# Kernel tuning notes

Measured on AMD Instinct MI355X. Metric: run time of the kernel, lower is better.

The kernel has to match this reference:

```python
import jax, jax.numpy as jnp
import numpy as np

M1, M2, M3 = 12, 12, 8
WIDTH = 32


def _spectral_conv(v, wr, wi):
    # v: [B, C, X, Y, T]; wr/wi: [4, Ci, Co, M1, M2, M3]
    B, C, X, Y, T = v.shape
    vft = jnp.fft.rfftn(v, axes=(-3, -2, -1))  # [B,C,X,Y,T//2+1] complex
    w = wr.astype(jnp.complex64) + 1j * wi.astype(jnp.complex64)
    mul = lambda blk, ww: jnp.einsum('bixyz,ioxyz->boxyz', blk, ww)
    out = jnp.zeros((B, wr.shape[2], X, Y, T // 2 + 1), dtype=vft.dtype)
    out = out.at[:, :, :M1, :M2, :M3].set(mul(vft[:, :, :M1, :M2, :M3], w[0]))
    out = out.at[:, :, -M1:, :M2, :M3].set(mul(vft[:, :, -M1:, :M2, :M3], w[1]))
    out = out.at[:, :, :M1, -M2:, :M3].set(mul(vft[:, :, :M1, -M2:, :M3], w[2]))
    out = out.at[:, :, -M1:, -M2:, :M3].set(mul(vft[:, :, -M1:, -M2:, :M3], w[3]))
    return jnp.fft.irfftn(out, s=(X, Y, T), axes=(-3, -2, -1))


def _conv1x1(v, w, b):
    # v: [B,C,X,Y,T]; w: [Co,Ci]; b: [Co]
    return jnp.einsum('bixyz,oi->boxyz', v, w) + b[None, :, None, None, None]


def setup_inputs() -> dict:
    key = jax.random.key(0)
    ks = jax.random.split(key, 24)
    B, X, Y, T = 8, 64, 64, 40
    W = WIDTH
    scale = 1.0 / (W * W)
    d = {}
    d['h'] = jax.random.normal(ks[0], (B, X, Y, T, 2), dtype=jnp.float32)
    d['x'] = jax.random.normal(ks[1], (B, X, Y, T, 3), dtype=jnp.float32)
    d['fc0_w'] = jax.random.normal(ks[2], (5, W), dtype=jnp.float32) * 0.3
    d['fc0_b'] = jnp.zeros((W,), dtype=jnp.float32)
    for i, name in enumerate(['sc0', 'sc1', 'sc3']):
        d[name + '_wr'] = scale * jax.random.uniform(ks[3 + 2 * i], (4, W, W, M1, M2, M3), dtype=jnp.float32)
        d[name + '_wi'] = scale * jax.random.uniform(ks[4 + 2 * i], (4, W, W, M1, M2, M3), dtype=jnp.float32)
    for i, name in enumerate(['w0', 'w1', 'w3']):
        d[name + '_w'] = jax.random.normal(ks[9 + 2 * i], (W, W), dtype=jnp.float32) * (1.0 / np.sqrt(W))
        d[name + '_b'] = jnp.zeros((W,), dtype=jnp.float32)
    d['fc1_w'] = jax.random.normal(ks[15], (W, 64), dtype=jnp.float32) * (1.0 / np.sqrt(W))
    d['fc1_b'] = jnp.zeros((64,), dtype=jnp.float32)
    d['fc2_w'] = jax.random.normal(ks[16], (64, 2), dtype=jnp.float32) * 0.125
    d['fc2_b'] = jnp.zeros((2,), dtype=jnp.float32)
    return d


def reference(h, x, fc0_w, fc0_b, sc0_wr, sc0_wi, sc1_wr, sc1_wi, sc3_wr, sc3_wi,
              w0_w, w0_b, w1_w, w1_b, w3_w, w3_b, fc1_w, fc1_b, fc2_w, fc2_b):
    v = jnp.concatenate((h, x), axis=-1)                 # [B,X,Y,T,5]
    v = v @ fc0_w + fc0_b                                # lift to width
    v = jnp.transpose(v, (0, 4, 1, 2, 3))                # [B,W,X,Y,T]
    v = jax.nn.gelu(_spectral_conv(v, sc0_wr, sc0_wi) + _conv1x1(v, w0_w, w0_b), approximate=False)
    v = jax.nn.gelu(_spectral_conv(v, sc1_wr, sc1_wi) + _conv1x1(v, w1_w, w1_b), approximate=False)
    v = _spectral_conv(v, sc3_wr, sc3_wi) + _conv1x1(v, w3_w, w3_b)
    v = jnp.transpose(v, (0, 2, 3, 4, 1))                # [B,X,Y,T,W]
    v = jax.nn.gelu(v @ fc1_w + fc1_b, approximate=False)
    return v @ fc2_w + fc2_b                             # [B,X,Y,T,2]
```

## Files before the change

kernel.cpp:

```cpp
#include <hip/hip_runtime.h>
#include <math.h>

#define BATCH 8
#define WID   32
#define NX    64
#define NY    64
#define NT    40
#define M1C   12
#define KT    8
#define KXC   24
#define KYC   24
#define NXY   (NX*NY)
#define NXYT  (NXY*NT)
#define NP    (BATCH*NXYT)

#define TWO_PI 6.283185307179586f

static __device__ __forceinline__ float gelu_f(float v){
  return 0.5f*v*(1.0f + erff(v*0.7071067811865476f));
}

static __device__ __forceinline__ void barrier_lds(){
  asm volatile("s_waitcnt lgkmcnt(0)\n\ts_barrier" ::: "memory");
}


__global__ __launch_bounds__(256) void k_fc0(const float* __restrict__ h, const float* __restrict__ x,
                                             const float* __restrict__ w, const float* __restrict__ b,
                                             float* __restrict__ V){
  __shared__ float sw[160], sb[32];
  int tid=threadIdx.x;
  if(tid<160) sw[tid]=w[tid];
  if(tid<32)  sb[tid]=b[tid];
  __syncthreads();
  int pl = tid>>3, q = tid&7;
  int p = blockIdx.x*32 + pl;
  float i0=h[(size_t)p*2], i1=h[(size_t)p*2+1];
  float i2=x[(size_t)p*3], i3=x[(size_t)p*3+1], i4=x[(size_t)p*3+2];
  int c0=q*4;
  float4 o;
  float* po=(float*)&o;
  #pragma unroll
  for(int u=0;u<4;u++){
    int c=c0+u;
    po[u] = sb[c] + i0*sw[c] + i1*sw[32+c] + i2*sw[64+c] + i3*sw[96+c] + i4*sw[128+c];
  }
  ((float4*)V)[(size_t)p*8 + q] = o;
}

__global__ __launch_bounds__(256) void k_fwd_ty(const float* __restrict__ V, float2* __restrict__ F2){
  __shared__ __align__(16) unsigned char smem[61696];
  float*  vt    = (float*)smem;
  float2* f2out = (float2*)smem;
  float2* twy   = (float2*)(smem + 49408);
  int tid = threadIdx.x;
  int b = blockIdx.x >> 6, x = blockIdx.x & 63;
  int c = tid & 31, k = tid >> 5;
  for(int i=tid;i<KYC*NY;i+=256){
    int ky=i/NY, y=i-ky*NY;
    int f = ky<M1C ? ky : ky+40;
    float ang = -TWO_PI*(float)((f*y)%NY)/(float)NY;
    twy[ky*NY+y] = make_float2(cosf(ang), sinf(ang));
  }
  float2 twr[NT];
  #pragma unroll
  for(int t=0;t<NT;t++){
    float ang = -TWO_PI*(float)((k*t)%NT)/(float)NT;
    twr[t] = make_float2(cosf(ang), sinf(ang));
  }
  float2 acc[KYC];
  #pragma unroll
  for(int ky=0;ky<KYC;ky++) acc[ky]=make_float2(0.f,0.f);
  const float4* src = (const float4*)(V + (size_t)(b*NX+x)*(NY*NT*WID));
  for(int g=0; g<8; g++){
    __syncthreads();
    #pragma unroll
    for(int r=0;r<10;r++) ((float4*)vt)[r*256+tid] = src[g*2560 + r*256 + tid];
    __syncthreads();
    for(int yl=0; yl<8; yl+=2){
      float sr0=0.f, si0=0.f, sr1=0.f, si1=0.f;
      const float* vp0 = vt + yl*1280 + c;
      const float* vp1 = vp0 + 1280;
      #pragma unroll
      for(int t=0;t<NT;t++){
        float2 w = twr[t];
        float v0 = vp0[t*32];
        float v1 = vp1[t*32];
        sr0 += v0*w.x; si0 += v0*w.y;
        sr1 += v1*w.x; si1 += v1*w.y;
      }
      int y = g*8 + yl;
      #pragma unroll
      for(int ky=0;ky<KYC;ky++){
        float4 wy = *(const float4*)&twy[ky*NY + y];
        acc[ky].x += sr0*wy.x - si0*wy.y + sr1*wy.z - si1*wy.w;
        acc[ky].y += sr0*wy.y + si0*wy.x + sr1*wy.w + si1*wy.z;
      }
    }
  }
  __syncthreads();
  #pragma unroll
  for(int ky=0;ky<KYC;ky++) f2out[c*193 + ky*KT + k] = acc[ky];
  __syncthreads();
  for(int i=tid;i<WID*KYC*KT;i+=256){
    int cc=i/192, e=i-cc*192;
    F2[((size_t)(b*WID+cc)*NX + x)*(KYC*KT) + e] = f2out[cc*193 + e];
  }
}

__global__ __launch_bounds__(256) void k_fwd_x(const float2* __restrict__ F2, float2* __restrict__ F3){
  __shared__ float2 tile[NX*KT];
  __shared__ float2 twi[KXC*65];
  int tid=threadIdx.x;
  int bc = blockIdx.x / KYC;
  int ky = blockIdx.x - bc*KYC;
  for(int i=tid;i<NX*KT;i+=256){
    int xx=i/KT, kt=i-xx*KT;
    tile[i] = F2[((size_t)bc*NX + xx)*(KYC*KT) + ky*KT + kt];
  }
  for(int i=tid;i<KXC*NX;i+=256){
    int kx=i/NX, xx=i-kx*NX;
    int f = kx<M1C ? kx : kx+40;
    float ang = -TWO_PI*(float)((f*xx)%NX)/(float)NX;
    twi[kx*65+xx] = make_float2(cosf(ang), sinf(ang));
  }
  __syncthreads();
  for(int item=tid; item<KXC*KT; item+=256){
    int kx=item/KT, kt=item-kx*KT;
    float sr=0.f, si=0.f;
    #pragma unroll 8
    for(int xx=0;xx<NX;xx++){
      float2 a = tile[xx*KT+kt];
      float2 w = twi[kx*65+xx];
      sr += a.x*w.x - a.y*w.y;
      si += a.x*w.y + a.y*w.x;
    }
    F3[(size_t)bc*(KXC*KYC*KT) + kx*(KYC*KT) + ky*KT + kt] = make_float2(sr,si);
  }
}

__global__ __launch_bounds__(256) void k_mix(const float2* __restrict__ F3, const float* __restrict__ wr,
                                             const float* __restrict__ wi, float2* __restrict__ F4){
  __shared__ float2 f3s[BATCH*WID*KT];
  int tid = threadIdx.x;
  int kx = blockIdx.x / KYC, ky = blockIdx.x - kx*KYC;
  int mode0 = blockIdx.x * KT;
  int xp = (kx>=M1C), yp = (ky>=M1C);
  int m1 = kx - M1C*xp, m2 = ky - M1C*yp;
  int blk = xp + 2*yp;
  for(int i=tid;i<1024;i+=256){
    int row=i>>2, q=i&3;
    ((float4*)f3s)[row*4+q] = ((const float4*)(F3 + (size_t)row*4608 + mode0))[q];
  }
  int o = tid>>3, kt = tid&7;
  size_t wbase = (size_t)blk*1179648 + (size_t)o*1152 + m1*96 + m2*8 + kt;
  float wre[WID], wim[WID];
  #pragma unroll
  for(int i=0;i<WID;i++){
    wre[i] = wr[wbase + (size_t)i*36864];
    wim[i] = wi[wbase + (size_t)i*36864];
  }
  __syncthreads();
  #pragma unroll
  for(int b=0;b<BATCH;b++){
    float ar=0.f, ai=0.f;
    #pragma unroll
    for(int i=0;i<WID;i++){
      float2 a = f3s[(b*WID+i)*KT + kt];
      ar += a.x*wre[i] - a.y*wim[i];
      ai += a.x*wim[i] + a.y*wre[i];
    }
    F4[(size_t)(b*WID+o)*4608 + mode0 + kt] = make_float2(ar,ai);
  }
}

__global__ __launch_bounds__(256) void k_inv_x(const float2* __restrict__ F4, float2* __restrict__ F2){
  __shared__ float2 tile[KXC*KT];
  __shared__ float2 twi[NX*25];
  int tid=threadIdx.x;
  int bc = blockIdx.x / KYC, ky = blockIdx.x - (blockIdx.x/KYC)*KYC;
  for(int i=tid;i<KXC*KT;i+=256){
    int kx=i/KT, kt=i-kx*KT;
    tile[i] = F4[(size_t)bc*4608 + kx*(KYC*KT) + ky*KT + kt];
  }
  for(int i=tid;i<NX*KXC;i+=256){
    int xx=i/KXC, kx=i-xx*KXC;
    int f = kx<M1C ? kx : kx+40;
    float ang = TWO_PI*(float)((f*xx)%NX)/(float)NX;
    twi[xx*25+kx] = make_float2(cosf(ang)*(1.0f/64.0f), sinf(ang)*(1.0f/64.0f));
  }
  __syncthreads();
  for(int item=tid; item<NX*KT; item+=256){
    int xx=item/KT, kt=item-xx*KT;
    float sr=0.f, si=0.f;
    #pragma unroll 8
    for(int kx=0;kx<KXC;kx++){
      float2 a = tile[kx*KT+kt];
      float2 w = twi[xx*25+kx];
      sr += a.x*w.x - a.y*w.y;
      si += a.x*w.y + a.y*w.x;
    }
    F2[((size_t)bc*NX + xx)*(KYC*KT) + ky*KT + kt] = make_float2(sr,si);
  }
}

template<bool GELU>
__global__ __launch_bounds__(256) void k_conv(const float2* __restrict__ F2, const float* __restrict__ wcv,
                                              const float* __restrict__ bcv, float* __restrict__ V){
  __shared__ __align__(16) unsigned char smem[24576];
  float*  vt0  = (float*)smem;
  float*  vt1  = (float*)(smem+5120);
  float2* ftc0 = (float2*)(smem+10240);
  float2* ftc1 = (float2*)(smem+12288);
  float2* twy  = (float2*)(smem+14336);
  float2* f2h  = (float2*)smem;

  int tid=threadIdx.x;
  int b  = blockIdx.x >> 7;
  int x  = (blockIdx.x >> 1) & 63;
  int y0 = (blockIdx.x & 1) * 32;
  int cid = tid & 31, ktid = tid >> 5;
  int oid = tid & 31, tg  = tid >> 5;

  float2 fr[KYC];
  #pragma unroll
  for(int half=0; half<2; half++){
    for(int i=tid;i<1536;i+=256){
      int cc=i/96, q=i-cc*96;
      ((float4*)f2h)[i] = *((const float4*)(F2 + ((size_t)(b*WID + half*16 + cc)*NX + x)*(KYC*KT)) + q);
    }
    __syncthreads();
    if((cid>>4) == half){
      const float2* fp = f2h + (cid&15)*192 + ktid;
      #pragma unroll
      for(int ky=0;ky<KYC;ky++) fr[ky] = fp[ky*8];
    }
    __syncthreads();
  }
  {
    float ts = (ktid==0 ? 1.0f : 2.0f) * (1.0f/(float)NT);
    #pragma unroll
    for(int ky=0;ky<KYC;ky++){ fr[ky].x *= ts; fr[ky].y *= ts; }
  }
  float wreg[WID];
  #pragma unroll
  for(int cc=0;cc<WID;cc++) wreg[cc] = wcv[oid*WID + cc];
  float breg = bcv[oid];
  float2 twtg[KT];
  #pragma unroll
  for(int k=0;k<KT;k++){
    float ang = 0.78539816339744831f*(float)((k*tg)&7);
    twtg[k] = make_float2(cosf(ang), sinf(ang));
  }
  for(int i=tid;i<32*KYC;i+=256){
    int yy=i/KYC, ky=i-yy*KYC;
    int f = ky<M1C ? ky : ky+40;
    float ang = TWO_PI*(float)((f*(y0+yy))%NY)/(float)NY;
    twy[i] = make_float2(cosf(ang)*(1.0f/64.0f), sinf(ang)*(1.0f/64.0f));
  }
  float* plane = V + (size_t)((b*NX+x)*NY + y0)*(NT*WID);
  const float4* gp = (const float4*)plane;
  bool has2 = tid < 64;
  float4 g0 = gp[tid];
  float4 g1 = has2 ? gp[256+tid] : make_float4(0,0,0,0);
  ((float4*)vt0)[tid] = g0;
  if(has2) ((float4*)vt0)[256+tid] = g1;
  __syncthreads();

  constexpr float CJ[KT][5] = {
    {1.f, 1.f,          1.f,          1.f,          1.f         },
    {1.f, 0.98768834f,  0.95105652f,  0.89100652f,  0.80901699f },
    {1.f, 0.95105652f,  0.80901699f,  0.58778525f,  0.30901699f },
    {1.f, 0.89100652f,  0.58778525f,  0.15643447f, -0.30901699f },
    {1.f, 0.80901699f,  0.30901699f, -0.30901699f, -0.80901699f },
    {1.f, 0.70710678f,  0.f,         -0.70710678f, -1.f         },
    {1.f, 0.58778525f, -0.30901699f, -0.95105652f, -0.80901699f },
    {1.f, 0.45399050f, -0.58778525f, -0.98768834f, -0.30901699f },
  };
  constexpr float SJ[KT][5] = {
    {0.f, 0.f,          0.f,          0.f,          0.f         },
    {0.f, 0.15643447f,  0.30901699f,  0.45399050f,  0.58778525f },
    {0.f, 0.30901699f,  0.58778525f,  0.80901699f,  0.95105652f },
    {0.f, 0.45399050f,  0.80901699f,  0.98768834f,  0.95105652f },
    {0.f, 0.58778525f,  0.95105652f,  0.95105652f,  0.58778525f },
    {0.f, 0.70710678f,  1.f,          0.70710678f,  0.f         },
    {0.f, 0.80901699f,  0.95105652f,  0.30901699f, -0.58778525f },
    {0.f, 0.89100652f,  0.80901699f, -0.15643447f, -0.95105652f },
  };

  for(int y=0;y<32;y++){
    if(y+1 < 32){
      g0 = gp[(size_t)(y+1)*320 + tid];
      if(has2) g1 = gp[(size_t)(y+1)*320 + 256 + tid];
    }
    float2* ftcb = (y&1) ? ftc1 : ftc0;
    {
      const float2* tw = twy + y*KYC;
      float sr=0.f, si=0.f;
      #pragma unroll
      for(int ky=0;ky<KYC;ky++){
        float2 w = tw[ky];
        float2 a = fr[ky];
        sr += a.x*w.x - a.y*w.y;
        si += a.x*w.y + a.y*w.x;
      }
      ftcb[ktid*32 + cid] = make_float2(sr,si);
    }
    barrier_lds();
    {
      float acc[5];
      #pragma unroll
      for(int j=0;j<5;j++) acc[j] = breg;
      #pragma unroll
      for(int k=0;k<KT;k++){
        float2 f = ftcb[k*32 + oid];
        float gx = f.x*twtg[k].x - f.y*twtg[k].y;
        float gy = f.x*twtg[k].y + f.y*twtg[k].x;
        #pragma unroll
        for(int j=0;j<5;j++) acc[j] += gx*CJ[k][j] - gy*SJ[k][j];
      }
      const float* vb = (y&1) ? vt1 : vt0;
      float* outp = plane + (size_t)y*(NT*WID);
      #pragma unroll
      for(int j=0;j<5;j++){
        int t = tg*5 + j;
        float a = acc[j];
        const float* vrow = vb + t*32;
        #pragma unroll
        for(int c4=0;c4<WID;c4+=4){
          float4 vv = *(const float4*)(vrow + c4);
          a += vv.x*wreg[c4] + vv.y*wreg[c4+1] + vv.z*wreg[c4+2] + vv.w*wreg[c4+3];
        }
        outp[t*32 + oid] = GELU ? gelu_f(a) : a;
      }
    }
    if(y+1 < 32){
      float* d = (y&1) ? vt0 : vt1;
      ((float4*)d)[tid] = g0;
      if(has2) ((float4*)d)[256+tid] = g1;
    }
  }
}

__global__ __launch_bounds__(256) void k_mlp(const float* __restrict__ V, const float* __restrict__ w1,
                                             const float* __restrict__ b1, const float* __restrict__ w2,
                                             const float* __restrict__ b2, float* __restrict__ out){
  __shared__ float sw1t[64*WID];
  __shared__ float sb1[64], sw2[128], sb2[2];
  int tid=threadIdx.x;
  for(int i=tid;i<64*WID;i+=256){ int j=i>>5, c=i&31; sw1t[i]=w1[c*64+j]; }
  if(tid<64) sb1[tid]=b1[tid];
  if(tid<128) sw2[tid]=w2[tid];
  if(tid<2) sb2[tid]=b2[tid];
  __syncthreads();
  size_t p0 = (size_t)blockIdx.x*1024 + (size_t)tid*4;
  float vv[128];
  const float4* vp = (const float4*)(V + p0*WID);
  #pragma unroll
  for(int q=0;q<32;q++) *((float4*)(vv+4*q)) = vp[q];
  float oa[8];
  #pragma unroll
  for(int pt=0;pt<4;pt++){ oa[2*pt]=sb2[0]; oa[2*pt+1]=sb2[1]; }
  #pragma unroll 4
  for(int j=0;j<64;j++){
    float a0=sb1[j], a1=a0, a2=a0, a3=a0;
    const float* wrow = sw1t + j*WID;
    #pragma unroll
    for(int c4=0;c4<WID;c4+=4){
      float4 w = *(const float4*)(wrow + c4);
      a0 += vv[     c4]*w.x + vv[     c4+1]*w.y + vv[     c4+2]*w.z + vv[     c4+3]*w.w;
      a1 += vv[32 + c4]*w.x + vv[32 + c4+1]*w.y + vv[32 + c4+2]*w.z + vv[32 + c4+3]*w.w;
      a2 += vv[64 + c4]*w.x + vv[64 + c4+1]*w.y + vv[64 + c4+2]*w.z + vv[64 + c4+3]*w.w;
      a3 += vv[96 + c4]*w.x + vv[96 + c4+1]*w.y + vv[96 + c4+2]*w.z + vv[96 + c4+3]*w.w;
    }
    a0=gelu_f(a0); a1=gelu_f(a1); a2=gelu_f(a2); a3=gelu_f(a3);
    float u0=sw2[2*j], u1=sw2[2*j+1];
    oa[0]+=a0*u0; oa[1]+=a0*u1; oa[2]+=a1*u0; oa[3]+=a1*u1;
    oa[4]+=a2*u0; oa[5]+=a2*u1; oa[6]+=a3*u0; oa[7]+=a3*u1;
  }
  float4* op = (float4*)(out + p0*2);
  op[0]=make_float4(oa[0],oa[1],oa[2],oa[3]);
  op[1]=make_float4(oa[4],oa[5],oa[6],oa[7]);
}

extern "C" void kernel_launch(void* const* d_in, const int* in_sizes, int n_in,
                              void* d_out, int out_size, void* d_ws, size_t ws_size,
                              hipStream_t stream){
  const float* h     = (const float*)d_in[0];
  const float* x     = (const float*)d_in[1];
  const float* fc0_w = (const float*)d_in[2];
  const float* fc0_b = (const float*)d_in[3];
  const float* scwr[3] = {(const float*)d_in[4], (const float*)d_in[6], (const float*)d_in[8]};
  const float* scwi[3] = {(const float*)d_in[5], (const float*)d_in[7], (const float*)d_in[9]};
  const float* cw[3]   = {(const float*)d_in[10], (const float*)d_in[12], (const float*)d_in[14]};
  const float* cb[3]   = {(const float*)d_in[11], (const float*)d_in[13], (const float*)d_in[15]};
  const float* fc1_w = (const float*)d_in[16];
  const float* fc1_b = (const float*)d_in[17];
  const float* fc2_w = (const float*)d_in[18];
  const float* fc2_b = (const float*)d_in[19];

  const size_t VSZ = (size_t)BATCH*WID*NXYT;
  float*  V  = (float*)d_ws;
  float2* F2 = (float2*)(V + VSZ);
  float2* F4 = F2 + (size_t)BATCH*WID*NX*KYC*KT;
  float2* F3 = (float2*)d_out;

  k_fc0<<<NP/32, 256, 0, stream>>>(h, x, fc0_w, fc0_b, V);
  for(int L=0; L<3; L++){
    k_fwd_ty<<<BATCH*NX, 256, 0, stream>>>(V, F2);
    k_fwd_x<<<(BATCH*WID)*KYC, 256, 0, stream>>>(F2, F3);
    k_mix<<<KXC*KYC, 256, 0, stream>>>(F3, scwr[L], scwi[L], F4);
    k_inv_x<<<(BATCH*WID)*KYC, 256, 0, stream>>>(F4, F2);
    if(L<2) k_conv<true ><<<BATCH*NX*2, 256, 0, stream>>>(F2, cw[L], cb[L], V);
    else    k_conv<false><<<BATCH*NX*2, 256, 0, stream>>>(F2, cw[L], cb[L], V);
  }
  k_mlp<<<NP/1024, 256, 0, stream>>>(V, fc1_w, fc1_b, fc2_w, fc2_b, (float*)d_out);
}
```

Baseline: 1.555 ms.

## Process two y-rows per iteration in k_conv with deeper register prefetch

```diff
diff --git a/kernel.cpp b/kernel.cpp
--- a/kernel.cpp
+++ b/kernel.cpp
@@ -207,12 +207,12 @@
 template<bool GELU>
 __global__ __launch_bounds__(256) void k_conv(const float2* __restrict__ F2, const float* __restrict__ wcv,
                                               const float* __restrict__ bcv, float* __restrict__ V){
-  __shared__ __align__(16) unsigned char smem[24576];
-  float*  vt0  = (float*)smem;
-  float*  vt1  = (float*)(smem+5120);
-  float2* ftc0 = (float2*)(smem+10240);
-  float2* ftc1 = (float2*)(smem+12288);
-  float2* twy  = (float2*)(smem+14336);
+  __shared__ __align__(16) unsigned char smem[34816];
+  float*  vtA  = (float*)smem;
+  float*  vtB  = (float*)(smem+10240);
+  float2* ftc0 = (float2*)(smem+20480);
+  float2* ftc1 = (float2*)(smem+24576);
+  float2* twy  = (float2*)(smem+28672);
   float2* f2h  = (float2*)smem;
 
   int tid=threadIdx.x;
@@ -260,11 +260,16 @@
   }
   float* plane = V + (size_t)((b*NX+x)*NY + y0)*(NT*WID);
   const float4* gp = (const float4*)plane;
-  bool has2 = tid < 64;
-  float4 g0 = gp[tid];
-  float4 g1 = has2 ? gp[256+tid] : make_float4(0,0,0,0);
-  ((float4*)vt0)[tid] = g0;
-  if(has2) ((float4*)vt0)[256+tid] = g1;
+  bool has3 = tid < 128;
+  {
+    float4 p0 = gp[tid], p1 = gp[256+tid];
+    float4 p2 = has3 ? gp[512+tid] : make_float4(0,0,0,0);
+    ((float4*)vtA)[tid] = p0;
+    ((float4*)vtA)[256+tid] = p1;
+    if(has3) ((float4*)vtA)[512+tid] = p2;
+  }
+  float4 rA = gp[640+tid], rB = gp[640+256+tid];
+  float4 rC = has3 ? gp[640+512+tid] : make_float4(0,0,0,0);
   __syncthreads();
 
   constexpr float CJ[KT][5] = {
@@ -288,39 +293,57 @@
     {0.f, 0.89100652f,  0.80901699f, -0.15643447f, -0.95105652f },
   };
 
-  for(int y=0;y<32;y++){
-    if(y+1 < 32){
-      g0 = gp[(size_t)(y+1)*320 + tid];
-      if(has2) g1 = gp[(size_t)(y+1)*320 + 256 + tid];
-    }
-    float2* ftcb = (y&1) ? ftc1 : ftc0;
+  #pragma unroll 1
+  for(int it=0; it<16; ++it){
+    float*  vcur = (it&1) ? vtB  : vtA;
+    float*  vnxt = (it&1) ? vtA  : vtB;
+    float2* fcur = (it&1) ? ftc1 : ftc0;
+    int yl = it*2;
     {
-      const float2* tw = twy + y*KYC;
-      float sr=0.f, si=0.f;
-      #pragma unroll
-      for(int ky=0;ky<KYC;ky++){
-        float2 w = tw[ky];
-        float2 a = fr[ky];
-        sr += a.x*w.x - a.y*w.y;
-        si += a.x*w.y + a.y*w.x;
+      const float2* tw0 = twy + (size_t)yl*KYC;
+      const float2* tw1 = tw0 + KYC;
+      float sr0=0.f, si0=0.f, sr1=0.f, si1=0.f;
+      #pragma unroll
+      for(int ky=0;ky<KYC;ky+=2){
+        float2 a  = fr[ky];
+        float2 b2 = fr[ky+1];
+        float4 w0 = *(const float4*)&tw0[ky];
+        float4 w1 = *(const float4*)&tw1[ky];
+        sr0 += a.x*w0.x - a.y*w0.y + b2.x*w0.z - b2.y*w0.w;
+        si0 += a.x*w0.y + a.y*w0.x + b2.x*w0.w + b2.y*w0.z;
+        sr1 += a.x*w1.x - a.y*w1.y + b2.x*w1.z - b2.y*w1.w;
+        si1 += a.x*w1.y + a.y*w1.x + b2.x*w1.w + b2.y*w1.z;
       }
-      ftcb[ktid*32 + cid] = make_float2(sr,si);
+      fcur[      ktid*32 + cid] = make_float2(sr0,si0);
+      fcur[256 + ktid*32 + cid] = make_float2(sr1,si1);
     }
     barrier_lds();
-    {
+    if(it+1 < 16){
+      ((float4*)vnxt)[tid] = rA;
+      ((float4*)vnxt)[256+tid] = rB;
+      if(has3) ((float4*)vnxt)[512+tid] = rC;
+    }
+    if(it+2 < 16){
+      const float4* q = gp + (size_t)(it+2)*640;
+      rA = q[tid]; rB = q[256+tid];
+      if(has3) rC = q[512+tid];
+    }
+    #pragma unroll
+    for(int yy=0; yy<2; yy++){
+      const float2* fsrc = fcur + yy*256;
+      const float*  vb   = vcur + yy*1280;
+      float* outp = plane + (size_t)(yl+yy)*(NT*WID);
       float acc[5];
       #pragma unroll
       for(int j=0;j<5;j++) acc[j] = breg;
       #pragma unroll
       for(int k=0;k<KT;k++){
-        float2 f = ftcb[k*32 + oid];
+        float2 f = fsrc[k*32 + oid];
         float gx = f.x*twtg[k].x - f.y*twtg[k].y;
         float gy = f.x*twtg[k].y + f.y*twtg[k].x;
         #pragma unroll
         for(int j=0;j<5;j++) acc[j] += gx*CJ[k][j] - gy*SJ[k][j];
       }
-      const float* vb = (y&1) ? vt1 : vt0;
-      float* outp = plane + (size_t)y*(NT*WID);
       #pragma unroll
       for(int j=0;j<5;j++){
         int t = tg*5 + j;
@@ -333,11 +356,6 @@
         }
         outp[t*32 + oid] = GELU ? gelu_f(a) : a;
       }
-    }
-    if(y+1 < 32){
-      float* d = (y&1) ? vt0 : vt1;
-      ((float4*)d)[tid] = g0;
-      if(has2) ((float4*)d)[256+tid] = g1;
     }
   }
 }
```

Result: no change. 1.555 ms (+0.0%).
